# Kernel optimization log

Measured on AMD Instinct MI355X. Metric: run time of the kernel, lower is better.

## Reference

```python
import jax, jax.numpy as jnp
import numpy as np

N_CAND = 21  # tf.linspace(0, 1, 21) candidate pool
SOFTMIN_TEMP = 100.0


def _tree_constants(max_depth: int):
    """Signed split->descendant matrix M (S,N) and node->parent one-hot P (N,N)."""
    n_splits = 2 ** max_depth - 1
    n_nodes = 2 ** (max_depth + 1) - 1
    M = np.zeros((n_splits, n_nodes), np.float32)
    for s in range(n_splits):
        for n in range(n_nodes):
            a = n
            while a > 0:
                p = (a - 1) // 2
                if p == s:
                    # left-subtree descendants get -1, right-subtree +1
                    M[s, n] = -1.0 if a == 2 * s + 1 else 1.0
                    break
                a = p
    P = np.zeros((n_nodes, n_nodes), np.float32)
    for i in range(1, n_nodes):
        P[i, (i - 1) // 2] = 1.0
    return jnp.asarray(M), jnp.asarray(P), n_splits, n_nodes


def setup_inputs() -> dict:
    key = jax.random.key(0)
    kx, kw, kb = jax.random.split(key, 3)
    B, F = 512, 512
    max_depth = 8
    n_splits = 2 ** max_depth - 1
    x = jax.random.normal(kx, (B, F), dtype=jnp.float32)
    # VarianceScaling(scale=2.0, mode='fan_in') ~ std sqrt(2/F)
    W = jax.random.normal(kw, (F, n_splits), dtype=jnp.float32) * np.sqrt(2.0 / F).astype(np.float32)
    # keras RandomNormal default stddev=0.05
    b = jax.random.normal(kb, (n_splits,), dtype=jnp.float32) * 0.05
    return {"x": x, "W": W, "b": b, "max_depth": max_depth}


def reference(x, W, b, max_depth):
    M, P, n_splits, n_nodes = _tree_constants(int(max_depth))
    # q per split, then min over ancestor splits (method 0)
    q_split = x @ W + b                                   # (B, S)
    q_bsn = q_split[:, :, None] * M[None] + 1.0 - jnp.abs(M)[None]  # (B, S, N)
    q_node = jnp.min(q_bsn, axis=1)                       # (B, N)

    a_cand = jnp.linspace(0.0, 1.0, N_CAND)               # (C,)
    qn = q_node[:, :, None]                               # (B, N, 1)
    sqr = jnp.where(a_cand <= qn + 0.5, (a_cand - (qn + 0.5)) ** 2, 0.0)
    # reg part sums over the size-1 leading axis of a -> just a^2 (reg_lambda=1.0 in call)
    g_a = 0.5 * a_cand ** 2 + 0.5 * jnp.sum(sqr, axis=0)  # (N, C)

    eye = jnp.eye(n_nodes, dtype=jnp.float32)

    def body(carry, _):
        n2g, _ = carry
        g_grp = n2g.T @ g_a                               # (N, C): group-summed objective
        w = jax.nn.softmax(-SOFTMIN_TEMP * g_grp, axis=1)
        a_grp = jnp.sum(a_cand * w, axis=1)               # (N,) soft argmin over candidates
        a_node = n2g @ a_grp                              # (N,) broadcast group value to nodes
        a_par = (P @ a_node)[1:]
        a_par = jnp.concatenate([jnp.ones((1,), a_node.dtype), a_par])
        viol = a_node - a_par
        t = jnp.argmax(viol)
        cond = (jnp.max(viol) <= 1e-8) & (t > 0)
        t_oh = jax.nn.one_hot(t, n_nodes, dtype=jnp.float32)
        p_oh = t_oh @ P
        n2g = n2g + jnp.where(cond, 1.0, 0.0) * jnp.outer(t_oh, p_oh - t_oh)
        return (n2g, a_node), None

    (_, a_node), _ = jax.lax.scan(body, (eye, jnp.zeros(n_nodes, jnp.float32)), None,
                                  length=n_nodes + 1)
    trajectory = jnp.clip(q_node, 0.0, a_node[None, :])   # (B, N)
    return trajectory
```

## Files before the change

kernel.cpp:

```cpp
#include <hip/hip_runtime.h>
#include <hip/hip_bf16.h>
#include <math.h>

#define BATCH 512
#define FDIM  512
#define NSPL  255
#define NNOD  511
#define NC    21


__global__ __launch_bounds__(256) void k_qgemm(const float* __restrict__ x,
                                               const float* __restrict__ W,
                                               float* __restrict__ partial,
                                               int fpc) {
  __shared__ float Ws[64 * 68];
  __shared__ float xT[64 * 68];
  const int tid = threadIdx.x;
  const int s0 = blockIdx.x * 64;
  const int b0 = blockIdx.y * 64;
  const int f0 = blockIdx.z * fpc;
  const int sx = tid & 15;
  const int by = tid >> 4;
  float acc[4][4];
#pragma unroll
  for (int i = 0; i < 4; ++i)
#pragma unroll
    for (int j = 0; j < 4; ++j) acc[i][j] = 0.f;

  for (int fc = f0; fc < f0 + fpc; fc += 64) {
    {
      int si = tid & 63, fr = tid >> 6;
#pragma unroll
      for (int r = 0; r < 16; ++r) {
        int fi = fr + r * 4;
        int s = s0 + si;
        Ws[fi * 68 + si] = (s < NSPL) ? W[(fc + fi) * NSPL + s] : 0.f;
      }
      int j = tid & 63, ir = tid >> 6;
#pragma unroll
      for (int r = 0; r < 16; ++r) {
        int i = ir + r * 4;
        xT[j * 68 + i] = x[(b0 + i) * FDIM + (fc + j)];
      }
    }
    __syncthreads();
#pragma unroll 8
    for (int f = 0; f < 64; ++f) {
      float4 av = *(const float4*)&Ws[f * 68 + sx * 4];
      float4 xv = *(const float4*)&xT[f * 68 + by * 4];
      const float a4[4] = {av.x, av.y, av.z, av.w};
      const float x4[4] = {xv.x, xv.y, xv.z, xv.w};
#pragma unroll
      for (int i = 0; i < 4; ++i)
#pragma unroll
        for (int j = 0; j < 4; ++j) acc[i][j] += a4[i] * x4[j];
    }
    __syncthreads();
  }

  float* pout = partial + (size_t)blockIdx.z * (256 * BATCH);
#pragma unroll
  for (int i = 0; i < 4; ++i) {
    int s = s0 + sx * 4 + i;
    if (s < NSPL) {
      float4 v = make_float4(acc[i][0], acc[i][1], acc[i][2], acc[i][3]);
      *(float4*)&pout[s * BATCH + b0 + by * 4] = v;
    }
  }
}

__global__ __launch_bounds__(256) void k_qreduce(const float* __restrict__ partial,
                                                 const float* __restrict__ bias,
                                                 float* __restrict__ qsT, int n) {
  int idx = blockIdx.x * 256 + threadIdx.x;
  if (idx >= NSPL * BATCH) return;
  int s = idx >> 9;
  float v = 0.f;
  for (int c = 0; c < n; ++c) v += partial[(size_t)c * (256 * BATCH) + idx];
  qsT[idx] = v + bias[s];
}

__global__ __launch_bounds__(256) void k_qsplitT_fb(const float* __restrict__ x,
                                                    const float* __restrict__ W,
                                                    const float* __restrict__ bias,
                                                    float* __restrict__ qsT) {
  const int s = threadIdx.x;
  const int b0 = blockIdx.x * 8;
  if (s >= NSPL) return;
  float acc0[8], acc1[8];
#pragma unroll
  for (int i = 0; i < 8; ++i) { acc0[i] = 0.f; acc1[i] = 0.f; }
#pragma unroll 2
  for (int f = 0; f < 256; ++f) {
    float w0 = W[f * NSPL + s];
    float w1 = W[(f + 256) * NSPL + s];
#pragma unroll
    for (int i = 0; i < 8; ++i) {
      acc0[i] += x[(b0 + i) * FDIM + f] * w0;
      acc1[i] += x[(b0 + i) * FDIM + f + 256] * w1;
    }
  }
  float bs = bias[s];
#pragma unroll
  for (int i = 0; i < 8; ++i) qsT[s * BATCH + b0 + i] = (acc0[i] + acc1[i]) + bs;
}

__device__ __forceinline__ float qnode_walk(const float* __restrict__ qsT, int n, int b) {
  float q = 1.0f;
  int a = n;
  while (a > 0) {
    int p = (a - 1) >> 1;
    float v = qsT[p * BATCH + b];
    q = fminf(q, (a & 1) ? -v : v);
    a = p;
  }
  return q;
}

__global__ __launch_bounds__(256) void k_ga(const float* __restrict__ qsT,
                                            float* __restrict__ ga,
                                            double* __restrict__ agrp0) {
  const int n = blockIdx.x;
  const int tid = threadIdx.x;
  __shared__ float qs[BATCH];
  __shared__ double part[4][NC];
  __shared__ float gaRow[NC];
#pragma unroll
  for (int rep = 0; rep < 2; ++rep) {
    int b = tid + rep * 256;
    qs[b] = qnode_walk(qsT, n, b);
  }
  __syncthreads();
  if (tid < 4 * NC) {
    int c = tid % NC, chunk = tid / NC;
    double ac = 0.05 * (double)c;
    double ssum = 0.0;
    int b0 = chunk * 128;
    for (int b = b0; b < b0 + 128; ++b) {
      float qh = qs[b] + 0.5f;
      double dqh = (double)qh;
      if (ac <= dqh) { double d = ac - dqh; ssum += d * d; }
    }
    part[chunk][c] = ssum;
  }
  __syncthreads();
  if (tid < NC) {
    double ac = 0.05 * (double)tid;
    double ssum = ((part[0][tid] + part[1][tid]) + part[2][tid]) + part[3][tid];
    float gv = (float)(0.5 * ac * ac + 0.5 * ssum);
    ga[n * NC + tid] = gv;
    gaRow[tid] = gv;
  }
  __syncthreads();
  if (tid == 0) {
    double z[NC], m = -1e300;
#pragma unroll
    for (int c = 0; c < NC; ++c) { z[c] = -100.0 * (double)gaRow[c]; m = fmax(m, z[c]); }
    double S = 0.0;
#pragma unroll
    for (int c = 0; c < NC; ++c) { z[c] = exp(z[c] - m); S += z[c]; }
    double A = 0.0;
#pragma unroll
    for (int c = 0; c < NC; ++c) A += (0.05 * (double)c) * (z[c] / S);
    agrp0[n] = A;
  }
}

__global__ __launch_bounds__(64) void k_scan(const float* __restrict__ ga_g,
                                             const double* __restrict__ agrp0,
                                             double* __restrict__ a_node_out) {
  __shared__ float gaS[NNOD * NC];
  __shared__ double agrp[512];
  __shared__ double anode[512];
  __shared__ float kfS[512];
  const int lane = threadIdx.x;

  {
    const float4* src = (const float4*)ga_g;
    float4* dst = (float4*)gaS;
    const int n4 = (NNOD * NC) / 4;
#pragma unroll 4
    for (int i = lane; i < n4; i += 64) dst[i] = src[i];
    if (lane < (NNOD * NC) - n4 * 4) gaS[n4 * 4 + lane] = ga_g[n4 * 4 + lane];
  }
  for (int i = lane; i < 512; i += 64) {
    agrp[i] = (i < NNOD) ? agrp0[i] : 0.0;
    anode[i] = 0.0;
    kfS[i] = 0.0f;
  }
  __syncthreads();

  int t = 0, p = 0;
  double areg[8];
  int iter = 0;
  for (;;) {
    if (iter > 0) {
      int j = lane >> 5, c = lane & 31;
      int g = j ? p : t;
      double z = -1e300;
      if (c < NC) {
        double acc = (1.0 - (double)kfS[g]) * (double)gaS[g * NC + c];
        int l = 2 * g + 1, r = 2 * g + 2;
        if (l < NNOD) acc = acc + (double)kfS[l] * (double)gaS[l * NC + c];
        if (r < NNOD) acc = acc + (double)kfS[r] * (double)gaS[r * NC + c];
        z = -100.0 * acc;
      }
      double m = z;
#pragma unroll
      for (int off = 16; off >= 1; off >>= 1) m = fmax(m, __shfl_xor(m, off, 32));
      double e = (c < NC) ? exp(z - m) : 0.0;
      double S = e;
#pragma unroll
      for (int off = 16; off >= 1; off >>= 1) S += __shfl_xor(S, off, 32);
      double term = (c < NC) ? (0.05 * (double)c) * (e / S) : 0.0;
#pragma unroll
      for (int off = 16; off >= 1; off >>= 1) term += __shfl_xor(term, off, 32);
      if (c == 0) agrp[g] = term;
      __syncthreads();
    }

#pragma unroll
    for (int u = 0; u < 8; ++u) {
      int n = lane + (u << 6);
      if (n < NNOD) {
        double kn = (double)kfS[n];
        double agn = agrp[n];
        double an;
        if (n == 0) an = agn;
        else an = kn * agrp[(n - 1) >> 1] + (1.0 - kn) * agn;
        areg[u] = an;
        anode[n] = an;
      }
    }
    __syncthreads();

    double bv = -1e300; int bi = 0x7fffffff;
#pragma unroll
    for (int u = 0; u < 8; ++u) {
      int n = lane + (u << 6);
      if (n < NNOD) {
        double ap = (n == 0) ? 1.0 : anode[(n - 1) >> 1];
        double vi = areg[u] - ap;
        if (vi > bv) { bv = vi; bi = n; }
      }
    }
#pragma unroll
    for (int off = 32; off >= 1; off >>= 1) {
      double ov = __shfl_xor(bv, off, 64);
      int oi = __shfl_xor(bi, off, 64);
      if (ov > bv || (ov == bv && oi < bi)) { bv = ov; bi = oi; }
    }

    bool cond = (bv <= 1e-8) && (bi > 0);
    if (!cond || iter == 511) break;
    t = bi; p = (t - 1) >> 1;
    if (lane == 0) kfS[t] += 1.0f;
    __syncthreads();
    ++iter;
  }

#pragma unroll
  for (int u = 0; u < 8; ++u) {
    int n = lane + (u << 6);
    if (n < NNOD) a_node_out[n] = areg[u];
  }
}

__global__ __launch_bounds__(256) void k_out(const float* __restrict__ qsT,
                                             const double* __restrict__ a_node,
                                             float* __restrict__ out) {
  __shared__ float col[NSPL];
  const int b = blockIdx.x;
  const int tid = threadIdx.x;
  if (tid < NSPL) col[tid] = qsT[tid * BATCH + b];
  __syncthreads();
#pragma unroll
  for (int rep = 0; rep < 2; ++rep) {
    int n = tid + rep * 256;
    if (n < NNOD) {
      float q = 1.0f;
      int a = n;
      while (a > 0) {
        int p = (a - 1) >> 1;
        float v = col[p];
        q = fminf(q, (a & 1) ? -v : v);
        a = p;
      }
      double r = fmin(fmax((double)q, 0.0), a_node[n]);
      out[(size_t)b * NNOD + n] = (float)r;
    }
  }
}

extern "C" void kernel_launch(void* const* d_in, const int* in_sizes, int n_in,
                              void* d_out, int out_size, void* d_ws, size_t ws_size,
                              hipStream_t stream) {
  (void)in_sizes; (void)n_in; (void)out_size;
  const float* x    = (const float*)d_in[0];
  const float* W    = (const float*)d_in[1];
  const float* bias = (const float*)d_in[2];
  float* out = (float*)d_out;

  char* ws = (char*)d_ws;
  const size_t PART_STRIDE = 256 * BATCH * sizeof(float);
  const size_t TAIL = 575488;

  int n = 8;
  while (n > 1 && (size_t)n * PART_STRIDE + TAIL > ws_size) n >>= 1;
  bool splitk_ok = ((size_t)n * PART_STRIDE + TAIL <= ws_size);

  size_t P = splitk_ok ? (size_t)n * PART_STRIDE : 0;
  float*  qsT    = (float*) (ws + P);
  float*  ga     = (float*) (ws + P + 524288);
  double* agrp0  = (double*)(ws + P + 567296);
  double* a_node = (double*)(ws + P + 571392);

  if (splitk_ok) {
    float* partial = (float*)ws;
    k_qgemm<<<dim3(4, 8, n), dim3(256), 0, stream>>>(x, W, partial, 512 / n);
    k_qreduce<<<dim3(510), dim3(256), 0, stream>>>(partial, bias, qsT, n);
  } else {
    k_qsplitT_fb<<<dim3(64), dim3(256), 0, stream>>>(x, W, bias, qsT);
  }
  k_ga<<<dim3(NNOD), dim3(256), 0, stream>>>(qsT, ga, agrp0);
  k_scan<<<dim3(1), dim3(64), 0, stream>>>(ga, agrp0, a_node);
  k_out<<<dim3(BATCH), dim3(256), 0, stream>>>(qsT, a_node, out);
}
```

Measured before the change: 93.80 us.

## Fuse split-K reduction into k_ga, store q_node, and replace k_out with a transpose clip

```diff
diff --git a/kernel.cpp b/kernel.cpp
--- a/kernel.cpp
+++ b/kernel.cpp
@@ -69,17 +69,6 @@
   }
 }
 
-__global__ __launch_bounds__(256) void k_qreduce(const float* __restrict__ partial,
-                                                 const float* __restrict__ bias,
-                                                 float* __restrict__ qsT, int n) {
-  int idx = blockIdx.x * 256 + threadIdx.x;
-  if (idx >= NSPL * BATCH) return;
-  int s = idx >> 9;
-  float v = 0.f;
-  for (int c = 0; c < n; ++c) v += partial[(size_t)c * (256 * BATCH) + idx];
-  qsT[idx] = v + bias[s];
-}
-
 __global__ __launch_bounds__(256) void k_qsplitT_fb(const float* __restrict__ x,
                                                     const float* __restrict__ W,
                                                     const float* __restrict__ bias,
@@ -105,32 +94,71 @@
   for (int i = 0; i < 8; ++i) qsT[s * BATCH + b0 + i] = (acc0[i] + acc1[i]) + bs;
 }
 
-__device__ __forceinline__ float qnode_walk(const float* __restrict__ qsT, int n, int b) {
-  float q = 1.0f;
-  int a = n;
-  while (a > 0) {
-    int p = (a - 1) >> 1;
-    float v = qsT[p * BATCH + b];
-    q = fminf(q, (a & 1) ? -v : v);
-    a = p;
-  }
-  return q;
-}
-
-__global__ __launch_bounds__(256) void k_ga(const float* __restrict__ qsT,
+__global__ __launch_bounds__(256) void k_ga(const float* __restrict__ src,
+                                            const float* __restrict__ bias,
+                                            int nchunks,
                                             float* __restrict__ ga,
-                                            double* __restrict__ agrp0) {
+                                            double* __restrict__ agrp0,
+                                            float* __restrict__ qnodeT) {
   const int n = blockIdx.x;
   const int tid = threadIdx.x;
+  __shared__ float anc[8][BATCH];
   __shared__ float qs[BATCH];
   __shared__ double part[4][NC];
   __shared__ float gaRow[NC];
+  __shared__ double zS[NC];
+  __shared__ double eS[NC];
+  __shared__ double mS;
+  __shared__ int pathS[8];
+  __shared__ int sgnS[8];
+  __shared__ int dS;
+
+  if (tid == 0) {
+    int a = n, d = 0;
+    while (a > 0) {
+      int p = (a - 1) >> 1;
+      pathS[d] = p;
+      sgnS[d] = a & 1;
+      ++d;
+      a = p;
+    }
+    dS = d;
+  }
+  __syncthreads();
+  const int d = dS;
+
+  for (int i = tid; i < d * 128; i += 256) {
+    int j = i >> 7, q4 = i & 127;
+    int s = pathS[j];
+    float4 v;
+    if (nchunks == 0) {
+      v = *(const float4*)&src[s * BATCH + q4 * 4];
+    } else {
+      v = make_float4(0.f, 0.f, 0.f, 0.f);
+      for (int z = 0; z < nchunks; ++z) {
+        float4 p = *(const float4*)&src[(size_t)z * (256 * BATCH) + s * BATCH + q4 * 4];
+        v.x += p.x; v.y += p.y; v.z += p.z; v.w += p.w;
+      }
+      float bs = bias[s];
+      v.x += bs; v.y += bs; v.z += bs; v.w += bs;
+    }
+    *(float4*)&anc[j][q4 * 4] = v;
+  }
+  __syncthreads();
+
 #pragma unroll
   for (int rep = 0; rep < 2; ++rep) {
     int b = tid + rep * 256;
-    qs[b] = qnode_walk(qsT, n, b);
-  }
-  __syncthreads();
+    float q = 1.0f;
+    for (int j = 0; j < d; ++j) {
+      float v = anc[j][b];
+      q = fminf(q, sgnS[j] ? -v : v);
+    }
+    qs[b] = q;
+    qnodeT[n * BATCH + b] = q;
+  }
+  __syncthreads();
+
   if (tid < 4 * NC) {
     int c = tid % NC, chunk = tid / NC;
     double ac = 0.05 * (double)c;
@@ -139,7 +167,7 @@
     for (int b = b0; b < b0 + 128; ++b) {
       float qh = qs[b] + 0.5f;
       double dqh = (double)qh;
-      if (ac <= dqh) { double d = ac - dqh; ssum += d * d; }
+      if (ac <= dqh) { double d2 = ac - dqh; ssum += d2 * d2; }
     }
     part[chunk][c] = ssum;
   }
@@ -152,16 +180,25 @@
     gaRow[tid] = gv;
   }
   __syncthreads();
+
+  if (tid < NC) zS[tid] = -100.0 * (double)gaRow[tid];
+  __syncthreads();
   if (tid == 0) {
-    double z[NC], m = -1e300;
-#pragma unroll
-    for (int c = 0; c < NC; ++c) { z[c] = -100.0 * (double)gaRow[c]; m = fmax(m, z[c]); }
+    double m = -1e300;
+#pragma unroll
+    for (int c = 0; c < NC; ++c) m = fmax(m, zS[c]);
+    mS = m;
+  }
+  __syncthreads();
+  if (tid < NC) eS[tid] = exp(zS[tid] - mS);
+  __syncthreads();
+  if (tid == 0) {
     double S = 0.0;
 #pragma unroll
-    for (int c = 0; c < NC; ++c) { z[c] = exp(z[c] - m); S += z[c]; }
+    for (int c = 0; c < NC; ++c) S += eS[c];
     double A = 0.0;
 #pragma unroll
-    for (int c = 0; c < NC; ++c) A += (0.05 * (double)c) * (z[c] / S);
+    for (int c = 0; c < NC; ++c) A += (0.05 * (double)c) * (eS[c] / S);
     agrp0[n] = A;
   }
 }
@@ -266,28 +303,28 @@
   }
 }
 
-__global__ __launch_bounds__(256) void k_out(const float* __restrict__ qsT,
-                                             const double* __restrict__ a_node,
-                                             float* __restrict__ out) {
-  __shared__ float col[NSPL];
-  const int b = blockIdx.x;
+__global__ __launch_bounds__(256) void k_clip(const float* __restrict__ qnodeT,
+                                              const double* __restrict__ a_node,
+                                              float* __restrict__ out) {
+  __shared__ float tile[64][65];
+  __shared__ double anS[64];
+  const int n0 = blockIdx.x * 64;
+  const int b0 = blockIdx.y * 64;
   const int tid = threadIdx.x;
-  if (tid < NSPL) col[tid] = qsT[tid * BATCH + b];
-  __syncthreads();
-#pragma unroll
-  for (int rep = 0; rep < 2; ++rep) {
-    int n = tid + rep * 256;
-    if (n < NNOD) {
-      float q = 1.0f;
-      int a = n;
-      while (a > 0) {
-        int p = (a - 1) >> 1;
-        float v = col[p];
-        q = fminf(q, (a & 1) ? -v : v);
-        a = p;
-      }
-      double r = fmin(fmax((double)q, 0.0), a_node[n]);
-      out[(size_t)b * NNOD + n] = (float)r;
+  if (tid < 64) anS[tid] = (n0 + tid < NNOD) ? a_node[n0 + tid] : 0.0;
+  for (int i = tid; i < 64 * 64; i += 256) {
+    int ni = i >> 6, bj = i & 63;
+    int nn = n0 + ni;
+    tile[ni][bj] = (nn < NNOD) ? qnodeT[nn * BATCH + b0 + bj] : 0.f;
+  }
+  __syncthreads();
+  for (int i = tid; i < 64 * 64; i += 256) {
+    int bi = i >> 6, nj = i & 63;
+    int nn = n0 + nj;
+    if (nn < NNOD) {
+      float q = tile[nj][bi];
+      double r = fmin(fmax((double)q, 0.0), anS[nj]);
+      out[(size_t)(b0 + bi) * NNOD + nn] = (float)r;
     }
   }
 }
@@ -303,26 +340,31 @@
 
   char* ws = (char*)d_ws;
   const size_t PART_STRIDE = 256 * BATCH * sizeof(float);
-  const size_t TAIL = 575488;
+  const size_t QN = 1048576;
+  const size_t GA = 43008;
+  const size_t AG = 4096;
+  const size_t AN = 4096;
+  const size_t TAIL = QN + GA + AG + AN;
 
   int n = 8;
   while (n > 1 && (size_t)n * PART_STRIDE + TAIL > ws_size) n >>= 1;
   bool splitk_ok = ((size_t)n * PART_STRIDE + TAIL <= ws_size);
 
-  size_t P = splitk_ok ? (size_t)n * PART_STRIDE : 0;
-  float*  qsT    = (float*) (ws + P);
-  float*  ga     = (float*) (ws + P + 524288);
-  double* agrp0  = (double*)(ws + P + 567296);
-  double* a_node = (double*)(ws + P + 571392);
+  size_t P = splitk_ok ? (size_t)n * PART_STRIDE : 524288;
+  float*  qnodeT = (float*) (ws + P);
+  float*  ga     = (float*) (ws + P + QN);
+  double* agrp0  = (double*)(ws + P + QN + GA);
+  double* a_node = (double*)(ws + P + QN + GA + AG);
 
   if (splitk_ok) {
     float* partial = (float*)ws;
     k_qgemm<<<dim3(4, 8, n), dim3(256), 0, stream>>>(x, W, partial, 512 / n);
-    k_qreduce<<<dim3(510), dim3(256), 0, stream>>>(partial, bias, qsT, n);
+    k_ga<<<dim3(NNOD), dim3(256), 0, stream>>>(partial, bias, n, ga, agrp0, qnodeT);
   } else {
+    float* qsT = (float*)ws;
     k_qsplitT_fb<<<dim3(64), dim3(256), 0, stream>>>(x, W, bias, qsT);
-  }
-  k_ga<<<dim3(NNOD), dim3(256), 0, stream>>>(qsT, ga, agrp0);
+    k_ga<<<dim3(NNOD), dim3(256), 0, stream>>>(qsT, bias, 0, ga, agrp0, qnodeT);
+  }
   k_scan<<<dim3(1), dim3(64), 0, stream>>>(ga, agrp0, a_node);
-  k_out<<<dim3(BATCH), dim3(256), 0, stream>>>(qsT, a_node, out);
-}
+  k_clip<<<dim3(8, 8), dim3(256), 0, stream>>>(qnodeT, a_node, out);
+}
```

Result: slower. 100.4 us (+7.0%).
